# Kernel optimization log

Hardware: AMD Instinct MI355X
Metric: run time of the kernel (lower is better)

## Reference

```python
import jax, jax.numpy as jnp
import numpy as np

B, T, D, H = 8, 1024, 1024, 16
HD = D // H  # per-head dim = 64


def setup_inputs() -> dict:
    key = jax.random.key(0)
    ks = jax.random.split(key, 9)
    s = 1.0 / np.sqrt(D)
    return {
        "x": jax.random.normal(ks[0], (B, T, D), dtype=jnp.float32),
        "y": jax.random.normal(ks[1], (B, T, D), dtype=jnp.float32),
        "Wq": jax.random.normal(ks[2], (D, D), dtype=jnp.float32) * s,
        "Wk": jax.random.normal(ks[3], (D, D), dtype=jnp.float32) * s,
        "Wv": jax.random.normal(ks[4], (D, D), dtype=jnp.float32) * s,
        "Wox": jax.random.normal(ks[5], (D, D), dtype=jnp.float32) * s,
        "box": jnp.zeros((D,), dtype=jnp.float32),
        "Woy": jax.random.normal(ks[6], (D, D), dtype=jnp.float32) * s,
        "boy": jnp.zeros((D,), dtype=jnp.float32),
    }


def _split_heads(t):
    # (B, T, D) -> (B, H, T, HD)
    return t.reshape(B, T, H, HD).transpose(0, 2, 1, 3)


def _merge_heads(t):
    # (B, H, T, HD) -> (B, T, D)
    return t.transpose(0, 2, 1, 3).reshape(B, T, D)


def reference(x, y, Wq, Wk, Wv, Wox, box, Woy, boy):
    # Shared Q/K/V projections applied cross-wise (torch Linear: t @ W.T)
    q_sx = _split_heads(y @ Wq.T)  # queries from y attend over x
    k_sx = _split_heads(x @ Wk.T)
    v_sx = _split_heads(x @ Wv.T)
    q_sy = _split_heads(x @ Wq.T)  # queries from x attend over y
    k_sy = _split_heads(y @ Wk.T)
    v_sy = _split_heads(y @ Wv.T)

    scale = jnp.sqrt(jnp.asarray(HD, dtype=x.dtype))
    scores_x = jnp.einsum('bhqd,bhkd->bhqk', q_sx, k_sx)
    scores_y = jnp.einsum('bhqd,bhkd->bhqk', q_sy, k_sy)
    # cat on head dim + reshape(B,2,H,T,T) + mean over dim 1 == per-head average
    attn = jax.nn.softmax((scores_x + scores_y) * (0.5 / scale), axis=-1)

    out1 = _merge_heads(jnp.einsum('bhqk,bhkd->bhqd', attn, v_sx))
    out2 = _merge_heads(jnp.einsum('bhqk,bhkd->bhqd', attn, v_sy))
    out1 = out1 @ Wox.T + box
    out2 = out2 @ Woy.T + boy
    return (out1, out2)
```

## Files before the change

### kernel.cpp

```cpp
#include <hip/hip_runtime.h>
#include <stdint.h>

#define DEV __device__ __forceinline__

typedef __bf16 bf16x8 __attribute__((ext_vector_type(8)));
typedef __bf16 bf16x4 __attribute__((ext_vector_type(4)));
typedef short s16x4 __attribute__((ext_vector_type(4)));
typedef float f32x4 __attribute__((ext_vector_type(4)));
typedef unsigned short u16;
typedef u16 u16x4v __attribute__((ext_vector_type(4)));
typedef u16 u16x8 __attribute__((ext_vector_type(8)));
typedef uint32_t u32;

static constexpr int Bb = 8, Tt = 1024, Dd = 1024, Hh = 16;
static constexpr int BT = Bb * Tt;

DEV u16 f2bf(float f) {
  u32 u = __float_as_uint(f);
  u32 r = (u + 0x7FFFu + ((u >> 16) & 1u)) >> 16;
  return (u16)r;
}
DEV u32 cvtpk(float lo, float hi) {
  u32 r;
  asm("v_cvt_pk_bf16_f32 %0, %1, %2" : "=v"(r) : "v"(lo), "v"(hi));
  return r;
}
DEV void gload_lds16(const void* g, void* lds) {
  __builtin_amdgcn_global_load_lds(
      (const __attribute__((address_space(1))) void*)g,
      (__attribute__((address_space(3))) void*)lds,
      16, 0, 0);
}
DEV f32x4 MFMA16(bf16x4 a, bf16x4 b, f32x4 c) {
#if __has_builtin(__builtin_amdgcn_mfma_f32_16x16x16_bf16)
  return __builtin_amdgcn_mfma_f32_16x16x16_bf16(a, b, c, 0, 0, 0);
#elif __has_builtin(__builtin_amdgcn_mfma_f32_16x16x16bf16_1k)
  union { bf16x4 b; s16x4 s; } ua, ub;
  ua.b = a; ub.b = b;
  return __builtin_amdgcn_mfma_f32_16x16x16bf16_1k(ua.s, ub.s, c, 0, 0, 0);
#else
  asm("v_mfma_f32_16x16x16_bf16 %0, %1, %2, %0" : "+v"(c) : "v"(a), "v"(b));
  return c;
#endif
}

__global__ __launch_bounds__(256) void k_cvt2(const float* __restrict__ x,
                                              const float* __restrict__ y,
                                              u16* __restrict__ xb, u16* __restrict__ yb) {
  const float* src = blockIdx.z ? y : x;
  u16* dst = blockIdx.z ? yb : xb;
  const int n8 = BT * Dd / 8;
  int i = blockIdx.x * blockDim.x + threadIdx.x;
  int stride = gridDim.x * blockDim.x;
  for (; i < n8; i += stride) {
    const float4* p = reinterpret_cast<const float4*>(src) + (size_t)i * 2;
    float4 a = p[0], b = p[1];
    u16x8 o;
    o[0] = f2bf(a.x); o[1] = f2bf(a.y); o[2] = f2bf(a.z); o[3] = f2bf(a.w);
    o[4] = f2bf(b.x); o[5] = f2bf(b.y); o[6] = f2bf(b.z); o[7] = f2bf(b.w);
    reinterpret_cast<u16x8*>(dst)[i] = o;
  }
}

__global__ __launch_bounds__(256) void k_cvt5(const float* __restrict__ a0,
                                              const float* __restrict__ a1,
                                              const float* __restrict__ a2,
                                              const float* __restrict__ a3,
                                              const float* __restrict__ a4,
                                              u16* __restrict__ Wb) {
  int z = blockIdx.z;
  const float* src = (z == 0) ? a0 : (z == 1) ? a1 : (z == 2) ? a2 : (z == 3) ? a3 : a4;
  u16* dst = Wb + (size_t)z * (Dd * Dd);
  int i = blockIdx.x * blockDim.x + threadIdx.x;
  const float4* p = reinterpret_cast<const float4*>(src) + (size_t)i * 2;
  float4 a = p[0], b = p[1];
  u16x8 o;
  o[0] = f2bf(a.x); o[1] = f2bf(a.y); o[2] = f2bf(a.z); o[3] = f2bf(a.w);
  o[4] = f2bf(b.x); o[5] = f2bf(b.y); o[6] = f2bf(b.z); o[7] = f2bf(b.w);
  reinterpret_cast<u16x8*>(dst)[i] = o;
}

template <int MODE, int GX, int GY>
__global__ __launch_bounds__(512, 2) void k_gemm256(
    const u16* __restrict__ xb, const u16* __restrict__ yb,
    const u16* __restrict__ W0,
    u16* __restrict__ Qb, u16* __restrict__ Kb, u16* __restrict__ Vtg,
    const float* __restrict__ bx, const float* __restrict__ by,
    float* __restrict__ out) {
  __shared__ alignas(16) u16 As[2][256 * 64];
  __shared__ alignas(16) u16 Bs[2][256 * 64];
  const int tid = threadIdx.x;
  const int l = tid & 63, wid = tid >> 6;
  const int wr = wid >> 2, wc = wid & 3;

  constexpr int NWG = GX * GY * 2;
  const int d0b = blockIdx.x;
  const int wk = (d0b & 7) * (NWG / 8) + (d0b >> 3);
  const int tz = wk / (GX * GY);
  const int rr = wk % (GX * GY);
  const int ty = rr / GX, tx = rr % GX;
  const int m0 = ty * 256, n0 = tx * 256;

  const u16* Ag;
  const u16* Wg;
  if constexpr (MODE == 0) {
    Ag = tz ? yb : xb;
    Wg = W0;
  } else {
    Ag = xb + tz * 64;
    Wg = W0 + (size_t)tz * (Dd * Dd);
  }

  auto stageA = [&](int buf, int kt, int half) {
#pragma unroll
    for (int i = 0; i < 2; ++i) {
      int idx = i * 512 + tid;
      int row = idx >> 3, P = idx & 7, G = P ^ (row & 7);
      const u16* src;
      if constexpr (MODE == 0) {
        src = Ag + (size_t)(m0 + half * 128 + row) * 1024 + kt * 64 + G * 8;
      } else {
        int m = m0 + half * 128 + row;
        src = Ag + ((size_t)((m >> 10) * 16 + kt) * 1024 + (m & 1023)) * 128 + G * 8;
      }
      gload_lds16(src, &As[buf][half * 8192 + idx * 8]);
    }
  };
  auto stageB = [&](int buf, int kt, int half) {
#pragma unroll
    for (int i = 0; i < 2; ++i) {
      int idx = i * 512 + tid;
      int row = idx >> 3, P = idx & 7, G = P ^ (row & 7);
      gload_lds16(Wg + (size_t)(n0 + half * 128 + row) * 1024 + kt * 64 + G * 8,
                  &Bs[buf][half * 8192 + idx * 8]);
    }
  };
  auto ldA = [&](int b, int m, int kk) -> bf16x8 {
    int row = wr * 128 + m * 16 + (l & 15);
    int P = (kk * 4 + (l >> 4)) ^ (row & 7);
    return *reinterpret_cast<const bf16x8*>(&As[b][row * 64 + P * 8]);
  };
  auto ldB = [&](int b, int n, int kk) -> bf16x8 {
    int row = wc * 64 + n * 16 + (l & 15);
    int P = (kk * 4 + (l >> 4)) ^ (row & 7);
    return *reinterpret_cast<const bf16x8*>(&Bs[b][row * 64 + P * 8]);
  };

  f32x4 acc[8][4] = {};

  stageA(0, 0, 0); stageB(0, 0, 0); stageA(0, 0, 1); stageB(0, 0, 1);
  asm volatile("s_waitcnt vmcnt(0)" ::: "memory");
  __builtin_amdgcn_s_barrier();

  for (int kt = 0; kt < 16; ++kt) {
    const int b = kt & 1, nb = b ^ 1;
    const bool pf = (kt < 15);
    bf16x8 bfr[4][2], afr[2][2];

#define QUAD(p)                                                                     \
  do {                                                                              \
    __builtin_amdgcn_s_barrier();                                                   \
    asm volatile("s_waitcnt lgkmcnt(0)" ::: "memory");                              \
    __builtin_amdgcn_sched_barrier(0);                                              \
    __builtin_amdgcn_s_setprio(1);                                                  \
    _Pragma("unroll") for (int mm = 0; mm < 2; ++mm)                                \
        _Pragma("unroll") for (int n = 0; n < 4; ++n)                               \
            _Pragma("unroll") for (int kk = 0; kk < 2; ++kk)                        \
                acc[2 * (p) + mm][n] = __builtin_amdgcn_mfma_f32_16x16x32_bf16(     \
                    afr[mm][kk], bfr[n][kk], acc[2 * (p) + mm][n], 0, 0, 0);        \
    __builtin_amdgcn_s_setprio(0);                                                  \
  } while (0)

#pragma unroll
    for (int n = 0; n < 4; ++n) { bfr[n][0] = ldB(b, n, 0); bfr[n][1] = ldB(b, n, 1); }
    afr[0][0] = ldA(b, 0, 0); afr[0][1] = ldA(b, 0, 1);
    afr[1][0] = ldA(b, 1, 0); afr[1][1] = ldA(b, 1, 1);
    if (pf) { stageA(nb, kt + 1, 0); stageB(nb, kt + 1, 0); }
    QUAD(0);
    __builtin_amdgcn_s_barrier();

    afr[0][0] = ldA(b, 2, 0); afr[0][1] = ldA(b, 2, 1);
    afr[1][0] = ldA(b, 3, 0); afr[1][1] = ldA(b, 3, 1);
    if (pf) { stageA(nb, kt + 1, 1); stageB(nb, kt + 1, 1); }
    QUAD(1);
    __builtin_amdgcn_s_barrier();

    afr[0][0] = ldA(b, 4, 0); afr[0][1] = ldA(b, 4, 1);
    afr[1][0] = ldA(b, 5, 0); afr[1][1] = ldA(b, 5, 1);
    QUAD(2);
    __builtin_amdgcn_s_barrier();

    afr[0][0] = ldA(b, 6, 0); afr[0][1] = ldA(b, 6, 1);
    afr[1][0] = ldA(b, 7, 0); afr[1][1] = ldA(b, 7, 1);
    QUAD(3);
    asm volatile("s_waitcnt vmcnt(0)" ::: "memory");
    __builtin_amdgcn_s_barrier();
#undef QUAD
  }

#pragma unroll
  for (int m = 0; m < 8; ++m)
#pragma unroll
    for (int n = 0; n < 4; ++n) {
      int rb = m0 + wr * 128 + m * 16 + (l >> 4) * 4;
      int col = n0 + wc * 64 + n * 16 + (l & 15);
      if constexpr (MODE == 0) {
        int proj = col >> 10;
        int slot = ((proj == 0) ? 1 : 0) ^ tz;
        int bh = ((rb >> 10) << 4) + ((col >> 6) & 15);
        int t0 = rb & 1023;
        int dc = col & 63;
        if (proj == 2) {
          int newoff = (t0 >> 5) * 32 + ((t0 >> 2) & 3) * 8 + ((t0 >> 4) & 1) * 4;
          u16x4v pk;
#pragma unroll
          for (int j = 0; j < 4; ++j) pk[j] = f2bf(acc[m][n][j]);
          *reinterpret_cast<u16x4v*>(Vtg + (size_t)bh * 131072 +
                                     (size_t)(slot * 64 + dc) * 1024 + newoff) = pk;
        } else {
          float sc = (proj == 0) ? 0.09016994f : 1.0f;
          u16* dstp = (proj ? Kb : Qb) + (size_t)bh * 131072 + (size_t)t0 * 128 + slot * 64 + dc;
#pragma unroll
          for (int j = 0; j < 4; ++j) dstp[(size_t)j * 128] = f2bf(acc[m][n][j] * sc);
        }
      } else {
        const float* bias = tz ? by : bx;
        float* dstp = out + (size_t)tz * BT * Dd;
        float bv = bias[col];
#pragma unroll
        for (int j = 0; j < 4; ++j)
          dstp[(size_t)(rb + j) * 1024 + col] = acc[m][n][j] + bv;
      }
    }
}

__global__ __launch_bounds__(256) void k_attn(const u16* __restrict__ Q,
                                              const u16* __restrict__ K,
                                              const u16* __restrict__ Vt,
                                              u16* __restrict__ O) {
  __shared__ alignas(16) u16 Ks[4 * 64 * 32];
  __shared__ alignas(16) u16 Vs[2 * 128 * 32];
  const int tid = threadIdx.x;
  const int l = tid & 63, w = tid >> 6;
  const int bid = blockIdx.x;
  const int xcd = bid & 7, li = bid >> 3;
  const int bh = xcd + 8 * (li >> 4);
  const int qx = li & 15;
  const int q0 = qx * 64 + w * 16;
  const size_t base = (size_t)bh * 131072;

  bf16x8 qf[4];
#pragma unroll
  for (int dc = 0; dc < 4; ++dc)
    qf[dc] = *reinterpret_cast<const bf16x8*>(
        Q + base + (size_t)(q0 + (l & 15)) * 128 + dc * 32 + (l >> 4) * 8);

  const u16* kp[4];
  const u16* vp[4];
#pragma unroll
  for (int r = 0; r < 4; ++r) {
    int idx = (r * 4 + w) * 64 + l;
    {
      int dc = idx >> 8, kv = (idx >> 2) & 63, pp = idx & 3, g = pp ^ ((kv >> 1) & 3);
      kp[r] = K + base + (size_t)kv * 128 + dc * 32 + g * 8;
    }
    {
      int c = idx >> 9, d = (idx >> 2) & 127, pp = idx & 3, g = pp ^ ((d >> 1) & 3);
      vp[r] = Vt + base + (size_t)d * 1024 + c * 32 + g * 8;
    }
  }
  const int koff = (l & 15) * 32 + (((l >> 4) ^ (((l & 15) >> 1) & 3))) * 8;
  const int voff = koff;

  float m_run = -3e38f, l_run = 0.f;
  f32x4 Oa[8] = {};

  for (int kv0 = 0; kv0 < 1024; kv0 += 64) {
#pragma unroll
    for (int r = 0; r < 4; ++r) {
      int chunk = r * 4 + w;
      gload_lds16(kp[r] + (size_t)kv0 * 128, &Ks[chunk * 512 + l * 8]);
      gload_lds16(vp[r] + kv0, &Vs[chunk * 512 + l * 8]);
    }
    __syncthreads();

    f32x4 S[4];
    __builtin_amdgcn_s_setprio(1);
#pragma unroll
    for (int t = 0; t < 4; ++t) {
      f32x4 s = {};
#pragma unroll
      for (int dc = 0; dc < 4; ++dc) {
        bf16x8 kb = *reinterpret_cast<const bf16x8*>(&Ks[dc * 2048 + t * 512 + koff]);
        s = __builtin_amdgcn_mfma_f32_16x16x32_bf16(kb, qf[dc], s, 0, 0, 0);
      }
      S[t] = s;
    }
    __builtin_amdgcn_s_setprio(0);

    float mx = fmaxf(fmaxf(fmaxf(S[0][0], S[0][1]), fmaxf(S[0][2], S[0][3])),
                     fmaxf(fmaxf(S[1][0], S[1][1]), fmaxf(S[1][2], S[1][3])));
    float mx2 = fmaxf(fmaxf(fmaxf(S[2][0], S[2][1]), fmaxf(S[2][2], S[2][3])),
                      fmaxf(fmaxf(S[3][0], S[3][1]), fmaxf(S[3][2], S[3][3])));
    mx = fmaxf(mx, mx2);
    mx = fmaxf(mx, __shfl_xor(mx, 16));
    mx = fmaxf(mx, __shfl_xor(mx, 32));

    const int grow = __any(mx > m_run + 11.0f);
    float mn = grow ? fmaxf(m_run, mx) : m_run;
    float rs = 0.f;
#pragma unroll
    for (int t = 0; t < 4; ++t)
#pragma unroll
      for (int j = 0; j < 4; ++j) {
        S[t][j] = __builtin_exp2f(S[t][j] - mn);
        rs += S[t][j];
      }
    rs += __shfl_xor(rs, 16);
    rs += __shfl_xor(rs, 32);
    if (grow) {
      float alpha = __builtin_exp2f(m_run - mn);
      m_run = mn;
      l_run = alpha * l_run + rs;
#pragma unroll
      for (int n = 0; n < 8; ++n) Oa[n] *= alpha;
    } else {
      l_run += rs;
    }

    union { u32 w2[2]; bf16x4 v; } pb[4];
#pragma unroll
    for (int t = 0; t < 4; ++t) {
      pb[t].w2[0] = cvtpk(S[t][0], S[t][1]);
      pb[t].w2[1] = cvtpk(S[t][2], S[t][3]);
    }

    asm volatile("s_nop 1");
    __builtin_amdgcn_s_setprio(1);
#pragma unroll
    for (int c = 0; c < 2; ++c)
#pragma unroll
      for (int n = 0; n < 8; ++n) {
        bf16x8 av = *reinterpret_cast<const bf16x8*>(&Vs[c * 4096 + n * 512 + voff]);
        bf16x4 a0 = __builtin_shufflevector(av, av, 0, 1, 2, 3);
        bf16x4 a1 = __builtin_shufflevector(av, av, 4, 5, 6, 7);
        Oa[n] = MFMA16(a0, pb[2 * c].v, Oa[n]);
        Oa[n] = MFMA16(a1, pb[2 * c + 1].v, Oa[n]);
      }
    __builtin_amdgcn_s_setprio(0);
    __syncthreads();
  }
  asm volatile("s_nop 7");

  float inv = 1.0f / l_run;
#pragma unroll
  for (int n = 0; n < 8; ++n) {
    u16x4v pk;
#pragma unroll
    for (int j = 0; j < 4; ++j) pk[j] = f2bf(Oa[n][j] * inv);
    *reinterpret_cast<u16x4v*>(
        O + base + (size_t)(q0 + (l & 15)) * 128 + n * 16 + (l >> 4) * 4) = pk;
  }
}

extern "C" void kernel_launch(void* const* d_in, const int* in_sizes, int n_in,
                              void* d_out, int out_size, void* d_ws, size_t ws_size,
                              hipStream_t stream) {
  const float* x   = (const float*)d_in[0];
  const float* y   = (const float*)d_in[1];
  const float* Wq  = (const float*)d_in[2];
  const float* Wk  = (const float*)d_in[3];
  const float* Wv  = (const float*)d_in[4];
  const float* Wox = (const float*)d_in[5];
  const float* box = (const float*)d_in[6];
  const float* Woy = (const float*)d_in[7];
  const float* boy = (const float*)d_in[8];

  u16* ws = (u16*)d_ws;
  size_t off = 0;
  u16* xb  = ws + off; off += (size_t)BT * Dd;
  u16* yb  = ws + off; off += (size_t)BT * Dd;
  u16* Wqb = ws + off; off += (size_t)Dd * Dd;
  u16* Wkb = ws + off; off += (size_t)Dd * Dd;
  u16* Wvb = ws + off; off += (size_t)Dd * Dd;
  u16* Woxb = ws + off; off += (size_t)Dd * Dd;
  u16* Woyb = ws + off; off += (size_t)Dd * Dd;
  (void)Wkb; (void)Wvb; (void)Woyb;
  const size_t attn_elems = (size_t)Bb * Hh * Tt * 128;
  u16* Qb = ws + off; off += attn_elems;
  u16* Kb = ws + off; off += attn_elems;
  u16* Vb = ws + off; off += attn_elems;
  u16* Ob = ws + off; off += attn_elems;

  k_cvt2<<<dim3(1024, 1, 2), dim3(256), 0, stream>>>(x, y, xb, yb);
  k_cvt5<<<dim3(512, 1, 5), dim3(256), 0, stream>>>(Wq, Wk, Wv, Wox, Woy, Wqb);

  k_gemm256<0, 12, 32><<<dim3(768), dim3(512), 0, stream>>>(
      xb, yb, Wqb, Qb, Kb, Vb, nullptr, nullptr, nullptr);

  k_attn<<<dim3(2048), dim3(256), 0, stream>>>(Qb, Kb, Vb, Ob);

  k_gemm256<1, 4, 32><<<dim3(256), dim3(512), 0, stream>>>(
      Ob, nullptr, Woxb, nullptr, nullptr, nullptr, box, boy, (float*)d_out);
}
```

Measured before the change: 292.8 us.

## Double-buffer K/V tiles in attention with 512-thread blocks covering 128 queries

The attention kernel now uses 8 waves per block, so each block handles 128 query rows and shares one K/V tile across twice as many waves. K/V staging is double-buffered: the next tile's global-to-LDS load is issued before computing on the current one, which leaves one barrier per iteration. The block-to-(batch,head) mapping is reordered, and the cross-lane max shuffle now runs only when the running max must grow. LDS use doubles to 64KB per block, which may limit occupancy.

New measurement: 276.2 us. 1.06x faster.

```diff
diff --git a/kernel.cpp b/kernel.cpp
--- a/kernel.cpp
+++ b/kernel.cpp
@@ -234,19 +234,19 @@
     }
 }
 
-__global__ __launch_bounds__(256) void k_attn(const u16* __restrict__ Q,
-                                              const u16* __restrict__ K,
-                                              const u16* __restrict__ Vt,
-                                              u16* __restrict__ O) {
-  __shared__ alignas(16) u16 Ks[4 * 64 * 32];
-  __shared__ alignas(16) u16 Vs[2 * 128 * 32];
+__global__ __launch_bounds__(512, 4) void k_attn(const u16* __restrict__ Q,
+                                                 const u16* __restrict__ K,
+                                                 const u16* __restrict__ Vt,
+                                                 u16* __restrict__ O) {
+  __shared__ alignas(16) u16 Ks[2][8192];
+  __shared__ alignas(16) u16 Vs[2][8192];
   const int tid = threadIdx.x;
   const int l = tid & 63, w = tid >> 6;
   const int bid = blockIdx.x;
   const int xcd = bid & 7, li = bid >> 3;
-  const int bh = xcd + 8 * (li >> 4);
-  const int qx = li & 15;
-  const int q0 = qx * 64 + w * 16;
+  const int bh = xcd + 8 * (li & 15);
+  const int qblk = li >> 4;
+  const int q0 = qblk * 128 + w * 16;
   const size_t base = (size_t)bh * 131072;
 
   bf16x8 qf[4];
@@ -255,34 +255,40 @@
     qf[dc] = *reinterpret_cast<const bf16x8*>(
         Q + base + (size_t)(q0 + (l & 15)) * 128 + dc * 32 + (l >> 4) * 8);
 
-  const u16* kp[4];
-  const u16* vp[4];
-#pragma unroll
-  for (int r = 0; r < 4; ++r) {
-    int idx = (r * 4 + w) * 64 + l;
+  const u16* kp[2];
+  const u16* vp[2];
+#pragma unroll
+  for (int i = 0; i < 2; ++i) {
+    int idx = i * 512 + tid;
     {
       int dc = idx >> 8, kv = (idx >> 2) & 63, pp = idx & 3, g = pp ^ ((kv >> 1) & 3);
-      kp[r] = K + base + (size_t)kv * 128 + dc * 32 + g * 8;
+      kp[i] = K + base + (size_t)kv * 128 + dc * 32 + g * 8;
     }
     {
       int c = idx >> 9, d = (idx >> 2) & 127, pp = idx & 3, g = pp ^ ((d >> 1) & 3);
-      vp[r] = Vt + base + (size_t)d * 1024 + c * 32 + g * 8;
-    }
-  }
+      vp[i] = Vt + base + (size_t)d * 1024 + c * 32 + g * 8;
+    }
+  }
+  const int i0 = tid * 8, i1 = (512 + tid) * 8;
+
   const int koff = (l & 15) * 32 + (((l >> 4) ^ (((l & 15) >> 1) & 3))) * 8;
-  const int voff = koff;
+
+  auto stage = [&](int buf, int kv0) {
+    gload_lds16(kp[0] + (size_t)kv0 * 128, &Ks[buf][i0]);
+    gload_lds16(kp[1] + (size_t)kv0 * 128, &Ks[buf][i1]);
+    gload_lds16(vp[0] + kv0, &Vs[buf][i0]);
+    gload_lds16(vp[1] + kv0, &Vs[buf][i1]);
+  };
 
   float m_run = -3e38f, l_run = 0.f;
   f32x4 Oa[8] = {};
 
-  for (int kv0 = 0; kv0 < 1024; kv0 += 64) {
-#pragma unroll
-    for (int r = 0; r < 4; ++r) {
-      int chunk = r * 4 + w;
-      gload_lds16(kp[r] + (size_t)kv0 * 128, &Ks[chunk * 512 + l * 8]);
-      gload_lds16(vp[r] + kv0, &Vs[chunk * 512 + l * 8]);
-    }
-    __syncthreads();
+  stage(0, 0);
+  __syncthreads();
+
+  for (int t16 = 0; t16 < 16; ++t16) {
+    const int cur = t16 & 1;
+    if (t16 < 15) stage(cur ^ 1, (t16 + 1) * 64);
 
     f32x4 S[4];
     __builtin_amdgcn_s_setprio(1);
@@ -291,23 +297,28 @@
       f32x4 s = {};
 #pragma unroll
       for (int dc = 0; dc < 4; ++dc) {
-        bf16x8 kb = *reinterpret_cast<const bf16x8*>(&Ks[dc * 2048 + t * 512 + koff]);
+        bf16x8 kb = *reinterpret_cast<const bf16x8*>(&Ks[cur][dc * 2048 + t * 512 + koff]);
         s = __builtin_amdgcn_mfma_f32_16x16x32_bf16(kb, qf[dc], s, 0, 0, 0);
       }
       S[t] = s;
     }
     __builtin_amdgcn_s_setprio(0);
 
-    float mx = fmaxf(fmaxf(fmaxf(S[0][0], S[0][1]), fmaxf(S[0][2], S[0][3])),
-                     fmaxf(fmaxf(S[1][0], S[1][1]), fmaxf(S[1][2], S[1][3])));
+    float mxl = fmaxf(fmaxf(fmaxf(S[0][0], S[0][1]), fmaxf(S[0][2], S[0][3])),
+                      fmaxf(fmaxf(S[1][0], S[1][1]), fmaxf(S[1][2], S[1][3])));
     float mx2 = fmaxf(fmaxf(fmaxf(S[2][0], S[2][1]), fmaxf(S[2][2], S[2][3])),
                       fmaxf(fmaxf(S[3][0], S[3][1]), fmaxf(S[3][2], S[3][3])));
-    mx = fmaxf(mx, mx2);
-    mx = fmaxf(mx, __shfl_xor(mx, 16));
-    mx = fmaxf(mx, __shfl_xor(mx, 32));
-
-    const int grow = __any(mx > m_run + 11.0f);
-    float mn = grow ? fmaxf(m_run, mx) : m_run;
+    mxl = fmaxf(mxl, mx2);
+
+    const int grow = __any(mxl > m_run + 11.0f);
+    float mn = m_run, alpha = 1.0f;
+    if (grow) {
+      float mx = fmaxf(mxl, __shfl_xor(mxl, 16));
+      mx = fmaxf(mx, __shfl_xor(mx, 32));
+      mn = fmaxf(m_run, mx);
+      alpha = __builtin_exp2f(m_run - mn);
+      m_run = mn;
+    }
     float rs = 0.f;
 #pragma unroll
     for (int t = 0; t < 4; ++t)
@@ -319,8 +330,6 @@
     rs += __shfl_xor(rs, 16);
     rs += __shfl_xor(rs, 32);
     if (grow) {
-      float alpha = __builtin_exp2f(m_run - mn);
-      m_run = mn;
       l_run = alpha * l_run + rs;
 #pragma unroll
       for (int n = 0; n < 8; ++n) Oa[n] *= alpha;
@@ -341,13 +350,14 @@
     for (int c = 0; c < 2; ++c)
 #pragma unroll
       for (int n = 0; n < 8; ++n) {
-        bf16x8 av = *reinterpret_cast<const bf16x8*>(&Vs[c * 4096 + n * 512 + voff]);
+        bf16x8 av = *reinterpret_cast<const bf16x8*>(&Vs[cur][c * 4096 + n * 512 + koff]);
         bf16x4 a0 = __builtin_shufflevector(av, av, 0, 1, 2, 3);
         bf16x4 a1 = __builtin_shufflevector(av, av, 4, 5, 6, 7);
         Oa[n] = MFMA16(a0, pb[2 * c].v, Oa[n]);
         Oa[n] = MFMA16(a1, pb[2 * c + 1].v, Oa[n]);
       }
     __builtin_amdgcn_s_setprio(0);
+
     __syncthreads();
   }
   asm volatile("s_nop 7");
@@ -398,7 +408,7 @@
   k_gemm256<0, 12, 32><<<dim3(768), dim3(512), 0, stream>>>(
       xb, yb, Wqb, Qb, Kb, Vb, nullptr, nullptr, nullptr);
 
-  k_attn<<<dim3(2048), dim3(256), 0, stream>>>(Qb, Kb, Vb, Ob);
+  k_attn<<<dim3(1024), dim3(512), 0, stream>>>(Qb, Kb, Vb, Ob);
 
   k_gemm256<1, 4, 32><<<dim3(256), dim3(512), 0, stream>>>(
       Ob, nullptr, Woxb, nullptr, nullptr, nullptr, box, boy, (float*)d_out);
```
